# Kernel tuning notes

Measured on AMD Instinct MI355X. Metric: run time of the kernel, lower is better.

## Reference

```python
import jax, jax.numpy as jnp
import numpy as np

B = 4096          # batch
F = 1024          # feature_count * embedding_dim
E = 16            # embedding_dim (domain embedding)
D = 8             # num_domains
T = F + E         # cross-net total dim
L = 3             # cross layers
EPS = 1e-5


def setup_inputs() -> dict:
    key = jax.random.key(0)
    ks = jax.random.split(key, 32)
    s = 0.02
    inp = {}
    inp["x"] = jax.random.normal(ks[0], (B, F), dtype=jnp.float32)
    inp["domain_ids"] = jax.random.randint(ks[1], (B,), 0, D)
    # partitioned normalization params
    inp["pn_weight"] = jnp.ones((D, F), jnp.float32)
    inp["pn_bias"] = jnp.zeros((D, F), jnp.float32)
    # domain embedding table
    inp["dom_emb"] = jax.random.normal(ks[2], (D, E), jnp.float32) * 0.1
    # cross network: L layers, each Linear(T->1, no bias) + additive bias vector
    inp["cross_w"] = jax.random.normal(ks[3], (L, T), jnp.float32) * s
    inp["cross_b"] = jnp.zeros((L, T), jnp.float32)
    # center MLP: T->512->256->128 (ReLU, ReLU, none)
    inp["cW1"] = jax.random.normal(ks[4], (T, 512), jnp.float32) * s
    inp["cb1"] = jnp.zeros((512,), jnp.float32)
    inp["cW2"] = jax.random.normal(ks[5], (512, 256), jnp.float32) * s
    inp["cb2"] = jnp.zeros((256,), jnp.float32)
    inp["cW3"] = jax.random.normal(ks[6], (256, 128), jnp.float32) * s
    inp["cb3"] = jnp.zeros((128,), jnp.float32)
    # per-domain nets: T->512->256->128; last bias initialized to domain_net_init_bias=1.0
    inp["dW1"] = jax.random.normal(ks[7], (D, T, 512), jnp.float32) * s
    inp["db1"] = jnp.zeros((D, 512), jnp.float32)
    inp["dW2"] = jax.random.normal(ks[8], (D, 512, 256), jnp.float32) * s
    inp["db2"] = jnp.zeros((D, 256), jnp.float32)
    inp["dW3"] = jax.random.normal(ks[9], (D, 256, 128), jnp.float32) * s
    inp["db3"] = jnp.ones((D, 128), jnp.float32)
    # final MLP: 128->64->1
    inp["fW1"] = jax.random.normal(ks[10], (128, 64), jnp.float32) * s
    inp["fb1"] = jnp.zeros((64,), jnp.float32)
    inp["fW2"] = jax.random.normal(ks[11], (64, 1), jnp.float32) * s
    inp["fb2"] = jnp.zeros((1,), jnp.float32)
    # auxiliary net: E->32->1
    inp["aW1"] = jax.random.normal(ks[12], (E, 32), jnp.float32) * s
    inp["ab1"] = jnp.zeros((32,), jnp.float32)
    inp["aW2"] = jax.random.normal(ks[13], (32, 1), jnp.float32) * s
    inp["ab2"] = jnp.zeros((1,), jnp.float32)
    return inp


def _forward(x, domain_ids, pn_weight, pn_bias, dom_emb, cross_w, cross_b,
             cW1, cb1, cW2, cb2, cW3, cb3,
             dW1, db1, dW2, db2, dW3, db3,
             fW1, fb1, fW2, fb2, aW1, ab1, aW2, ab2):
    # --- PartitionedNormalization: per-sample LayerNorm stats + domain-indexed affine ---
    mean = jnp.mean(x, axis=1, keepdims=True)
    var = jnp.mean((x - mean) ** 2, axis=1, keepdims=True)  # unbiased=False
    normed = (x - mean) / jnp.sqrt(var + EPS)
    normed = normed * pn_weight[domain_ids] + pn_bias[domain_ids]

    xd = dom_emb[domain_ids]                    # (B, E)
    x0 = jnp.concatenate([normed, xd], axis=1)  # (B, T)

    # --- CrossNetworkWithDomain ---
    xc = x0
    for i in range(L):
        proj = xc @ cross_w[i]                  # (B,)
        xc = x0 * proj[:, None] + cross_b[i] + xc

    # --- center MLP ---
    h = jax.nn.relu(xc @ cW1 + cb1)
    h = jax.nn.relu(h @ cW2 + cb2)
    h_center = h @ cW3 + cb3                    # (B, 128)

    # --- domain-specific nets: run all D nets, select per-sample ---
    a = jax.nn.relu(jnp.einsum('bi,dio->bdo', xc, dW1) + db1[None])   # (B, D, 512)
    a = jax.nn.relu(jnp.einsum('bdi,dio->bdo', a, dW2) + db2[None])   # (B, D, 256)
    a = jnp.einsum('bdi,dio->bdo', a, dW3) + db3[None]                # (B, D, 128)
    h_domain = a[jnp.arange(a.shape[0]), domain_ids]                  # (B, 128)

    # --- STAR fusion (tanh) ---
    fused = h_center * jnp.tanh(h_domain)

    # --- final MLP + auxiliary net ---
    main_logits = jax.nn.relu(fused @ fW1 + fb1) @ fW2 + fb2          # (B, 1)
    aux_logits = jax.nn.relu(xd @ aW1 + ab1) @ aW2 + ab2              # (B, 1)
    return jax.nn.sigmoid(main_logits + aux_logits)


def reference(x, domain_ids, pn_weight, pn_bias, dom_emb, cross_w, cross_b,
              cW1, cb1, cW2, cb2, cW3, cb3,
              dW1, db1, dW2, db2, dW3, db3,
              fW1, fb1, fW2, fb2, aW1, ab1, aW2, ab2):
    return _forward(x, domain_ids, pn_weight, pn_bias, dom_emb, cross_w, cross_b,
                    cW1, cb1, cW2, cb2, cW3, cb3,
                    dW1, db1, dW2, db2, dW3, db3,
                    fW1, fb1, fW2, fb2, aW1, ab1, aW2, ab2)
```

## Files before the change

### kernel.cpp

```cpp
#include <hip/hip_runtime.h>
#include <math.h>
#include <stdint.h>

#define BATCH 4096
#define FEAT  1024
#define EDIM  16
#define NDOM  8
#define TDIM  1040
#define KP1   1088
#define NLAYER 3
#define EPSV  1e-5f

typedef __attribute__((ext_vector_type(8))) short bf16x8;
typedef __attribute__((ext_vector_type(4))) float f32x4;

__device__ __forceinline__ unsigned short f2bf(float f) {
    union { float f; unsigned int u; } v; v.f = f;
    unsigned int u = v.u;
    return (unsigned short)((u + 0x7fffu + ((u >> 16) & 1u)) >> 16);
}
__device__ __forceinline__ float bf2f(unsigned short u) {
    union { unsigned int u; float f; } v; v.u = ((unsigned int)u) << 16; return v.f;
}
__device__ __forceinline__ void gload_lds16(const void* g, void* l) {
    __builtin_amdgcn_global_load_lds(
        (const __attribute__((address_space(1))) void*)(g),
        (__attribute__((address_space(3))) void*)(l), 16, 0, 0);
}

#define T_W1 136
#define T_W2 32
#define T_W3 8
#define NCONV (T_W1*9 + T_W2*9 + T_W3*9)

__global__ __launch_bounds__(256) void front(
    const int* __restrict__ dom, int* __restrict__ perm, int* __restrict__ starts,
    const float* __restrict__ cW1, const float* __restrict__ dW1,
    const float* __restrict__ cW2, const float* __restrict__ dW2,
    const float* __restrict__ cW3, const float* __restrict__ dW3,
    unsigned short* __restrict__ Wc1b, unsigned short* __restrict__ Wd1b,
    unsigned short* __restrict__ Wc2b, unsigned short* __restrict__ Wd2b,
    unsigned short* __restrict__ Wc3b, unsigned short* __restrict__ Wd3b,
    const float* __restrict__ x,
    const float* __restrict__ pnw, const float* __restrict__ pnb,
    const float* __restrict__ demb,
    const float* __restrict__ crw, const float* __restrict__ crb,
    const float* __restrict__ aW1, const float* __restrict__ ab1,
    const float* __restrict__ aW2, const float* __restrict__ ab2,
    unsigned short* __restrict__ XCb, float* __restrict__ auxg) {
    int b = blockIdx.x;
    int t = threadIdx.x;

    if (b < NCONV) {
        __shared__ float tile[64][65];
        const float* src; unsigned short* dst; int K, N, Kp, rr;
        if (b < T_W1)            { src = cW1; dst = Wc1b; K = TDIM; N = 512; Kp = KP1; rr = b; }
        else if (b < T_W1*9)     { int r = b - T_W1; int z = r / T_W1; rr = r % T_W1;
                                   src = dW1 + (size_t)z * TDIM * 512; dst = Wd1b + (size_t)z * 512 * KP1;
                                   K = TDIM; N = 512; Kp = KP1; }
        else if (b < T_W1*9+T_W2)   { src = cW2; dst = Wc2b; K = 512; N = 256; Kp = 512; rr = b - T_W1*9; }
        else if (b < T_W1*9+T_W2*9) { int r = b - (T_W1*9+T_W2); int z = r / T_W2; rr = r % T_W2;
                                   src = dW2 + (size_t)z * 512 * 256; dst = Wd2b + (size_t)z * 256 * 512;
                                   K = 512; N = 256; Kp = 512; }
        else if (b < T_W1*9+T_W2*9+T_W3) { src = cW3; dst = Wc3b; K = 256; N = 128; Kp = 256; rr = b - (T_W1*9+T_W2*9); }
        else                     { int r = b - (T_W1*9+T_W2*9+T_W3); int z = r / T_W3; rr = r % T_W3;
                                   src = dW3 + (size_t)z * 256 * 128; dst = Wd3b + (size_t)z * 128 * 256;
                                   K = 256; N = 128; Kp = 256; }
        int kt = Kp >> 6;
        int kb = rr % kt, nb = rr / kt;
        int k0 = kb * 64, n0 = nb * 64;
        #pragma unroll
        for (int i = 0; i < 4; i++) {
            int flat = t + i * 256;
            int kr = flat >> 4, c4 = flat & 15;
            int k = k0 + kr;
            float4 v = make_float4(0.f, 0.f, 0.f, 0.f);
            if (k < K) v = *(const float4*)(src + (size_t)k * N + n0 + c4 * 4);
            tile[kr][c4 * 4 + 0] = v.x;
            tile[kr][c4 * 4 + 1] = v.y;
            tile[kr][c4 * 4 + 2] = v.z;
            tile[kr][c4 * 4 + 3] = v.w;
        }
        __syncthreads();
        #pragma unroll
        for (int i = 0; i < 4; i++) {
            int flat = t + i * 256;
            int n = flat >> 4, kg = flat & 15;
            ushort4 sv;
            sv.x = f2bf(tile[kg * 4 + 0][n]);
            sv.y = f2bf(tile[kg * 4 + 1][n]);
            sv.z = f2bf(tile[kg * 4 + 2][n]);
            sv.w = f2bf(tile[kg * 4 + 3][n]);
            *(ushort4*)(dst + (size_t)(n0 + n) * Kp + k0 + kg * 4) = sv;
        }
        return;
    }
    if (b == NCONV) {
        __shared__ int cnt[NDOM];
        __shared__ int off[NDOM];
        if (t < NDOM) cnt[t] = 0;
        __syncthreads();
        for (int i = t; i < BATCH; i += 256) atomicAdd(&cnt[dom[i]], 1);
        __syncthreads();
        if (t == 0) {
            int s = 0;
            for (int d = 0; d < NDOM; d++) { off[d] = s; starts[d] = s; s += cnt[d]; }
            starts[NDOM] = s;
        }
        __syncthreads();
        for (int i = t; i < BATCH; i += 256) {
            int p = atomicAdd(&off[dom[i]], 1);
            perm[p] = i;
        }
        return;
    }

    int w = t >> 6, lane = t & 63;
    int row = (b - NCONV - 1) * 4 + w;
    int d = dom[row];

    float4 X[4];
    #pragma unroll
    for (int j = 0; j < 4; j++)
        X[j] = *(const float4*)(x + (size_t)row * FEAT + 4 * lane + 256 * j);

    float s = 0.f, ss = 0.f;
    #pragma unroll
    for (int j = 0; j < 4; j++) {
        s  += X[j].x + X[j].y + X[j].z + X[j].w;
        ss += X[j].x*X[j].x + X[j].y*X[j].y + X[j].z*X[j].z + X[j].w*X[j].w;
    }
    #pragma unroll
    for (int m = 1; m < 64; m <<= 1) {
        s  += __shfl_xor(s,  m);
        ss += __shfl_xor(ss, m);
    }
    float mean = s / (float)FEAT;
    float var  = ss / (float)FEAT - mean * mean;
    float rstd = rsqrtf(var + EPSV);

    float4 x0[4], xc[4];
    #pragma unroll
    for (int j = 0; j < 4; j++) {
        float4 wv = *(const float4*)(pnw + (size_t)d * FEAT + 4 * lane + 256 * j);
        float4 bv = *(const float4*)(pnb + (size_t)d * FEAT + 4 * lane + 256 * j);
        x0[j].x = (X[j].x - mean) * rstd * wv.x + bv.x;
        x0[j].y = (X[j].y - mean) * rstd * wv.y + bv.y;
        x0[j].z = (X[j].z - mean) * rstd * wv.z + bv.z;
        x0[j].w = (X[j].w - mean) * rstd * wv.w + bv.w;
        xc[j] = x0[j];
    }
    float x0e = 0.f, xce = 0.f;
    if (lane < EDIM) { x0e = demb[d * EDIM + lane]; xce = x0e; }

    #pragma unroll
    for (int l = 0; l < NLAYER; l++) {
        const float* wl = crw + l * TDIM;
        const float* bl = crb + l * TDIM;
        float partial = 0.f;
        #pragma unroll
        for (int j = 0; j < 4; j++) {
            float4 wv = *(const float4*)(wl + 4 * lane + 256 * j);
            partial += xc[j].x*wv.x + xc[j].y*wv.y + xc[j].z*wv.z + xc[j].w*wv.w;
        }
        if (lane < EDIM) partial += xce * wl[FEAT + lane];
        #pragma unroll
        for (int m = 1; m < 64; m <<= 1) partial += __shfl_xor(partial, m);
        float proj = partial;
        #pragma unroll
        for (int j = 0; j < 4; j++) {
            float4 bv = *(const float4*)(bl + 4 * lane + 256 * j);
            xc[j].x = fmaf(x0[j].x, proj, bv.x + xc[j].x);
            xc[j].y = fmaf(x0[j].y, proj, bv.y + xc[j].y);
            xc[j].z = fmaf(x0[j].z, proj, bv.z + xc[j].z);
            xc[j].w = fmaf(x0[j].w, proj, bv.w + xc[j].w);
        }
        if (lane < EDIM) xce = fmaf(x0e, proj, bl[FEAT + lane] + xce);
    }

    #pragma unroll
    for (int j = 0; j < 4; j++) {
        ushort4 sv;
        sv.x = f2bf(xc[j].x); sv.y = f2bf(xc[j].y);
        sv.z = f2bf(xc[j].z); sv.w = f2bf(xc[j].w);
        *(ushort4*)(XCb + (size_t)row * KP1 + 4 * lane + 256 * j) = sv;
    }
    XCb[(size_t)row * KP1 + FEAT + lane] = (lane < EDIM) ? f2bf(xce) : 0;

    float h = (lane < 32) ? ab1[lane] : 0.f;
    #pragma unroll
    for (int e = 0; e < EDIM; e++) {
        float ev = __shfl(xce, e);
        if (lane < 32) h = fmaf(ev, aW1[e * 32 + lane], h);
    }
    float c = (lane < 32) ? fmaxf(h, 0.f) * aW2[lane] : 0.f;
    #pragma unroll
    for (int m = 1; m < 64; m <<= 1) c += __shfl_xor(c, m);
    if (lane == 0) auxg[row] = c + ab2[0];
}

__global__ __launch_bounds__(256) void gemm_l1_fused(
    const unsigned short* __restrict__ A,
    const unsigned short* __restrict__ Wc,
    const unsigned short* __restrict__ Wd,
    const float* __restrict__ bc, const float* __restrict__ bd,
    unsigned short* __restrict__ Cc, unsigned short* __restrict__ Cd,
    const int* __restrict__ starts, const int* __restrict__ perm) {
    __shared__ short As[2][64 * 64];
    __shared__ short Bs[2][128 * 64];

    int xb = blockIdx.x;
    int d = xb >> 4, sl = xb & 15;
    int ds = starts[d], de = starts[d + 1];
    int m0 = ds + sl * 64;
    if (m0 >= de) return;
    int mEnd = de;
    int n0 = blockIdx.y * 64;

    int tid = threadIdx.x;
    int w = tid >> 6, lane = tid & 63;
    int lr = lane & 15, q = lane >> 4;

    const unsigned short* pA[2]; int sA[2];
    const unsigned short* pB[4]; int sB[4];
    #pragma unroll
    for (int i = 0; i < 2; i++) {
        int seg = i * 4 + w;
        int ch = seg * 64 + lane;
        int loc = ch >> 3, c = ch & 7;
        int mm = m0 + loc; if (mm > mEnd - 1) mm = mEnd - 1;
        int rowp = perm[mm];
        pA[i] = A + (size_t)rowp * KP1 + ((c ^ (loc & 7)) << 3);
        sA[i] = seg * 512;
    }
    #pragma unroll
    for (int i = 0; i < 4; i++) {
        int seg = i * 4 + w;
        int ch = seg * 64 + lane;
        int loc = ch >> 3, c = ch & 7;
        const unsigned short* base = (loc < 64)
            ? (Wc + (size_t)(n0 + loc) * KP1)
            : (Wd + ((size_t)d * 512 + n0 + (loc - 64)) * KP1);
        pB[i] = base + ((c ^ (loc & 7)) << 3);
        sB[i] = seg * 512;
    }

    f32x4 acc[4][2];
    #pragma unroll
    for (int i = 0; i < 4; i++)
        #pragma unroll
        for (int j = 0; j < 2; j++)
            acc[i][j] = (f32x4){0.f, 0.f, 0.f, 0.f};

    #pragma unroll
    for (int i = 0; i < 2; i++) gload_lds16(pA[i], As[0] + sA[i]);
    #pragma unroll
    for (int i = 0; i < 4; i++) gload_lds16(pB[i], Bs[0] + sB[i]);
    __syncthreads();

    #pragma unroll 1
    for (int ks = 0; ks < KP1 / 64; ks++) {
        int cur = ks & 1, nxt = cur ^ 1;
        if (ks < KP1 / 64 - 1) {
            int k0 = (ks + 1) * 64;
            #pragma unroll
            for (int i = 0; i < 2; i++) gload_lds16(pA[i] + k0, As[nxt] + sA[i]);
            #pragma unroll
            for (int i = 0; i < 4; i++) gload_lds16(pB[i] + k0, Bs[nxt] + sB[i]);
        }
        #pragma unroll
        for (int half = 0; half < 2; half++) {
            int cc = half * 4 + q;
            bf16x8 af[4], bf[2];
            #pragma unroll
            for (int i = 0; i < 4; i++) {
                int m = i * 16 + lr;
                af[i] = *(const bf16x8*)(As[cur] + m * 64 + ((cc ^ (m & 7)) << 3));
            }
            #pragma unroll
            for (int j = 0; j < 2; j++) {
                int n = w * 32 + j * 16 + lr;
                bf[j] = *(const bf16x8*)(Bs[cur] + n * 64 + ((cc ^ (n & 7)) << 3));
            }
            #pragma unroll
            for (int i = 0; i < 4; i++)
                #pragma unroll
                for (int j = 0; j < 2; j++)
                    acc[i][j] = __builtin_amdgcn_mfma_f32_16x16x32_bf16(
                        af[i], bf[j], acc[i][j], 0, 0, 0);
        }
        __syncthreads();
    }

    int chain = w >> 1, hn = w & 1;
    const float* bias = chain ? (bd + d * 512) : bc;
    unsigned short* C = chain ? Cd : Cc;
    #pragma unroll
    for (int i = 0; i < 4; i++) {
        #pragma unroll
        for (int j = 0; j < 2; j++) {
            int col = n0 + hn * 32 + j * 16 + lr;
            float bvv = bias[col];
            int rowb = m0 + i * 16 + q * 4;
            #pragma unroll
            for (int r = 0; r < 4; r++) {
                int row = rowb + r;
                if (row >= mEnd) continue;
                C[(size_t)row * 512 + col] = f2bf(fmaxf(acc[i][j][r] + bvv, 0.f));
            }
        }
    }
}

__global__ __launch_bounds__(256) void tail_fused(
    const unsigned short* __restrict__ H1c, const unsigned short* __restrict__ H1d,
    const unsigned short* __restrict__ Wc2, const unsigned short* __restrict__ Wd2,
    const float* __restrict__ cb2v, const float* __restrict__ db2v,
    const unsigned short* __restrict__ Wc3, const unsigned short* __restrict__ Wd3,
    const float* __restrict__ cb3v, const float* __restrict__ db3v,
    const float* __restrict__ fW1, const float* __restrict__ fb1,
    const float* __restrict__ fW2, const float* __restrict__ fb2,
    const float* __restrict__ auxg, const int* __restrict__ perm,
    const int* __restrict__ starts, float* __restrict__ out) {

    __shared__ __align__(16) char smem[98304];
    short* Bsb[2] = { (short*)smem, (short*)(smem + 32768) };
    short* Asb[2] = { (short*)(smem + 65536), (short*)(smem + 69632) };
    short* H2    = (short*)(smem + 73728);
    short* fused = (short*)(smem + 90112);

    int y = blockIdx.x;
    int d = y & 7, sl = y >> 3;
    int ds = starts[d], de = starts[d + 1];
    int m0 = ds + sl * 32;
    if (m0 >= de) return;
    int mEnd = de;

    int tid = threadIdx.x;
    int w = tid >> 6, lane = tid & 63;
    int lr = lane & 15, q = lane >> 4;

    int bn = w * 8 + (lane >> 3);
    int sw = ((lane & 7) ^ (bn & 7)) << 3;
    int rowA = m0 + bn; if (rowA > mEnd - 1) rowA = mEnd - 1;

    const unsigned short* pA0  = H1c + (size_t)rowA * 512 + sw;
    const unsigned short* pA1  = H1d + (size_t)rowA * 512 + sw;
    const unsigned short* pW20 = Wc2 + (size_t)bn * 512 + sw;
    const unsigned short* pW21 = Wd2 + (size_t)d * 256 * 512 + (size_t)bn * 512 + sw;
    const unsigned short* pW30 = Wc3 + (size_t)bn * 256 + sw;
    const unsigned short* pW31 = Wd3 + (size_t)d * 128 * 256 + (size_t)bn * 256 + sw;

    auto stage_l2 = [&](int c, int k0, int pb) {
        const unsigned short* pa = c ? pA1 : pA0;
        const unsigned short* pw = c ? pW21 : pW20;
        gload_lds16(pa + k0, Asb[pb] + w * 512);
        #pragma unroll
        for (int i = 0; i < 8; i++)
            gload_lds16(pw + (size_t)i * 32 * 512 + k0, Bsb[pb] + (i * 4 + w) * 512);
    };
    auto stage_l3 = [&](int c, int k0, int pb) {
        const unsigned short* pw = c ? pW31 : pW30;
        #pragma unroll
        for (int i = 0; i < 4; i++)
            gload_lds16(pw + (size_t)i * 32 * 256 + k0, Bsb[pb] + (i * 4 + w) * 512);
    };

    stage_l2(0, 0, 0);
    __syncthreads();

    #pragma unroll
    for (int c = 0; c < 2; c++) {
        f32x4 acc2[2][4];
        #pragma unroll
        for (int i = 0; i < 2; i++)
            #pragma unroll
            for (int j = 0; j < 4; j++) acc2[i][j] = (f32x4){0.f, 0.f, 0.f, 0.f};

        #pragma unroll
        for (int it = 0; it < 8; it++) {
            int t = c * 12 + it;
            int pb = t & 1, pn = pb ^ 1;
            if (it < 7) stage_l2(c, (it + 1) * 64, pn);
            else        stage_l3(c, 0, pn);

            #pragma unroll
            for (int half = 0; half < 2; half++) {
                int cc = half * 4 + q;
                bf16x8 af[2], bf[4];
                #pragma unroll
                for (int i = 0; i < 2; i++) {
                    int m = i * 16 + lr;
                    af[i] = *(const bf16x8*)(Asb[pb] + m * 64 + ((cc ^ (m & 7)) << 3));
                }
                #pragma unroll
                for (int j = 0; j < 4; j++) {
                    int n = w * 64 + j * 16 + lr;
                    bf[j] = *(const bf16x8*)(Bsb[pb] + n * 64 + ((cc ^ (n & 7)) << 3));
                }
                #pragma unroll
                for (int i = 0; i < 2; i++)
                    #pragma unroll
                    for (int j = 0; j < 4; j++)
                        acc2[i][j] = __builtin_amdgcn_mfma_f32_16x16x32_bf16(
                            af[i], bf[j], acc2[i][j], 0, 0, 0);
            }
            __syncthreads();
        }

        const float* b2 = c ? (db2v + d * 256) : cb2v;
        #pragma unroll
        for (int i = 0; i < 2; i++)
            #pragma unroll
            for (int j = 0; j < 4; j++) {
                int col = w * 64 + j * 16 + lr;
                float bv = b2[col];
                int cch = col >> 3;
                #pragma unroll
                for (int r = 0; r < 4; r++) {
                    int row = i * 16 + q * 4 + r;
                    int pc = (cch & 24) | ((cch ^ (row & 7)) & 7);
                    float v = fmaxf(acc2[i][j][r] + bv, 0.f);
                    H2[row * 256 + pc * 8 + (col & 7)] = (short)f2bf(v);
                }
            }
        __syncthreads();

        f32x4 acc3[2][2];
        #pragma unroll
        for (int i = 0; i < 2; i++)
            #pragma unroll
            for (int j = 0; j < 2; j++) acc3[i][j] = (f32x4){0.f, 0.f, 0.f, 0.f};

        #pragma unroll
        for (int it = 0; it < 4; it++) {
            int t = c * 12 + 8 + it;
            int pb = t & 1, pn = pb ^ 1;
            if (it < 3)      stage_l3(c, (it + 1) * 64, pn);
            else if (c == 0) stage_l2(1, 0, pn);

            #pragma unroll
            for (int half = 0; half < 2; half++) {
                int cc = half * 4 + q;
                int C = it * 8 + cc;
                bf16x8 af[2], bf[2];
                #pragma unroll
                for (int i = 0; i < 2; i++) {
                    int m = i * 16 + lr;
                    int pcm = (C & 24) | ((C ^ (m & 7)) & 7);
                    af[i] = *(const bf16x8*)(H2 + m * 256 + pcm * 8);
                }
                #pragma unroll
                for (int j = 0; j < 2; j++) {
                    int n = w * 32 + j * 16 + lr;
                    bf[j] = *(const bf16x8*)(Bsb[pb] + n * 64 + ((cc ^ (n & 7)) << 3));
                }
                #pragma unroll
                for (int i = 0; i < 2; i++)
                    #pragma unroll
                    for (int j = 0; j < 2; j++)
                        acc3[i][j] = __builtin_amdgcn_mfma_f32_16x16x32_bf16(
                            af[i], bf[j], acc3[i][j], 0, 0, 0);
            }
            __syncthreads();
        }

        const float* b3 = c ? (db3v + d * 128) : cb3v;
        #pragma unroll
        for (int i = 0; i < 2; i++)
            #pragma unroll
            for (int j = 0; j < 2; j++) {
                int col = w * 32 + j * 16 + lr;
                float bv = b3[col];
                int cch = col >> 3;
                #pragma unroll
                for (int r = 0; r < 4; r++) {
                    int row = i * 16 + q * 4 + r;
                    int pc = (cch & 8) | ((cch ^ (row & 7)) & 7);
                    int idx = row * 128 + pc * 8 + (col & 7);
                    if (c == 0) {
                        fused[idx] = (short)f2bf(acc3[i][j][r] + bv);
                    } else {
                        float cv = bf2f((unsigned short)fused[idx]);
                        fused[idx] = (short)f2bf(cv * tanhf(acc3[i][j][r] + bv));
                    }
                }
            }
        __syncthreads();
    }

    short* Bsf = Bsb[0];
    float* Ls  = (float*)Asb[0];
    for (int s2 = tid; s2 < 1024; s2 += 256) {
        int n = s2 >> 4, cch = s2 & 15;
        bf16x8 vv;
        #pragma unroll
        for (int kk = 0; kk < 8; kk++)
            vv[kk] = (short)f2bf(fW1[(cch * 8 + kk) * 64 + n]);
        int pc = (cch & 8) | ((cch ^ (n & 7)) & 7);
        *(bf16x8*)(Bsf + n * 128 + pc * 8) = vv;
    }
    __syncthreads();

    int wm = w >> 1, wn = w & 1;
    f32x4 acc2f[2];
    #pragma unroll
    for (int j = 0; j < 2; j++) acc2f[j] = (f32x4){0.f, 0.f, 0.f, 0.f};
    #pragma unroll
    for (int g = 0; g < 4; g++) {
        int cc = g * 4 + q;
        int m = wm * 16 + lr;
        int pcm = (cc & 8) | ((cc ^ (m & 7)) & 7);
        bf16x8 af = *(const bf16x8*)(fused + m * 128 + pcm * 8);
        #pragma unroll
        for (int j = 0; j < 2; j++) {
            int n = wn * 32 + j * 16 + lr;
            int pcn = (cc & 8) | ((cc ^ (n & 7)) & 7);
            bf16x8 bf = *(const bf16x8*)(Bsf + n * 128 + pcn * 8);
            acc2f[j] = __builtin_amdgcn_mfma_f32_16x16x32_bf16(af, bf, acc2f[j], 0, 0, 0);
        }
    }

    float w2v[2], b1v[2];
    #pragma unroll
    for (int j = 0; j < 2; j++) {
        int col = wn * 32 + j * 16 + lr;
        w2v[j] = fW2[col];
        b1v[j] = fb1[col];
    }
    float rowv[4];
    #pragma unroll
    for (int r = 0; r < 4; r++) {
        float v = 0.f;
        #pragma unroll
        for (int j = 0; j < 2; j++)
            v += fmaxf(acc2f[j][r] + b1v[j], 0.f) * w2v[j];
        v += __shfl_xor(v, 1);
        v += __shfl_xor(v, 2);
        v += __shfl_xor(v, 4);
        v += __shfl_xor(v, 8);
        rowv[r] = v;
    }
    if (wn == 0 && lr == 0) {
        #pragma unroll
        for (int r = 0; r < 4; r++)
            Ls[wm * 16 + q * 4 + r] = rowv[r];
    }
    __syncthreads();
    if (wn == 1 && lr == 0) {
        float b2 = fb2[0];
        #pragma unroll
        for (int r = 0; r < 4; r++) {
            int row = wm * 16 + q * 4 + r;
            int p = m0 + row;
            if (p < mEnd) {
                int orow = perm[p];
                float logit = Ls[row] + rowv[r] + b2 + auxg[orow];
                out[orow] = 1.f / (1.f + expf(-logit));
            }
        }
    }
}

extern "C" void kernel_launch(void* const* d_in, const int* in_sizes, int n_in,
                              void* d_out, int out_size, void* d_ws, size_t ws_size,
                              hipStream_t stream) {
    (void)in_sizes; (void)n_in; (void)out_size; (void)ws_size;

    const float* x    = (const float*)d_in[0];
    const int*   dom  = (const int*)  d_in[1];
    const float* pnw  = (const float*)d_in[2];
    const float* pnb  = (const float*)d_in[3];
    const float* demb = (const float*)d_in[4];
    const float* crw  = (const float*)d_in[5];
    const float* crb  = (const float*)d_in[6];
    const float* cW1  = (const float*)d_in[7];
    const float* cb1  = (const float*)d_in[8];
    const float* cW2  = (const float*)d_in[9];
    const float* cb2  = (const float*)d_in[10];
    const float* cW3  = (const float*)d_in[11];
    const float* cb3  = (const float*)d_in[12];
    const float* dW1  = (const float*)d_in[13];
    const float* db1  = (const float*)d_in[14];
    const float* dW2  = (const float*)d_in[15];
    const float* db2  = (const float*)d_in[16];
    const float* dW3  = (const float*)d_in[17];
    const float* db3  = (const float*)d_in[18];
    const float* fW1  = (const float*)d_in[19];
    const float* fb1  = (const float*)d_in[20];
    const float* fW2  = (const float*)d_in[21];
    const float* fb2  = (const float*)d_in[22];
    const float* aW1  = (const float*)d_in[23];
    const float* ab1  = (const float*)d_in[24];
    const float* aW2  = (const float*)d_in[25];
    const float* ab2  = (const float*)d_in[26];
    float* out = (float*)d_out;

    char* base = (char*)d_ws;
    size_t o = 0;
    auto alloc = [&](size_t bytes) { char* p = base + o; o += (bytes + 255) & ~size_t(255); return p; };

    int* perm   = (int*)alloc(BATCH * 4);
    int* starts = (int*)alloc((NDOM + 1) * 4);
    float* auxg = (float*)alloc(BATCH * 4);
    unsigned short* XCb  = (unsigned short*)alloc((size_t)BATCH * KP1 * 2);
    unsigned short* H1c  = (unsigned short*)alloc((size_t)BATCH * 512 * 2);
    unsigned short* H1d  = (unsigned short*)alloc((size_t)BATCH * 512 * 2);
    unsigned short* Wc1b = (unsigned short*)alloc((size_t)512 * KP1 * 2);
    unsigned short* Wd1b = (unsigned short*)alloc((size_t)NDOM * 512 * KP1 * 2);
    unsigned short* Wc2b = (unsigned short*)alloc((size_t)256 * 512 * 2);
    unsigned short* Wd2b = (unsigned short*)alloc((size_t)NDOM * 256 * 512 * 2);
    unsigned short* Wc3b = (unsigned short*)alloc((size_t)128 * 256 * 2);
    unsigned short* Wd3b = (unsigned short*)alloc((size_t)NDOM * 128 * 256 * 2);

    front<<<NCONV + 1 + BATCH / 4, 256, 0, stream>>>(
        dom, perm, starts, cW1, dW1, cW2, dW2, cW3, dW3,
        Wc1b, Wd1b, Wc2b, Wd2b, Wc3b, Wd3b,
        x, pnw, pnb, demb, crw, crb, aW1, ab1, aW2, ab2, XCb, auxg);

    gemm_l1_fused<<<dim3(NDOM * 16, 8), 256, 0, stream>>>(
        XCb, Wc1b, Wd1b, cb1, db1, H1c, H1d, starts, perm);

    tail_fused<<<NDOM * 128, 256, 0, stream>>>(
        H1c, H1d, Wc2b, Wd2b, cb2, db2, Wc3b, Wd3b, cb3, db3,
        fW1, fb1, fW2, fb2, auxg, perm, starts, out);
}
```

Baseline: 197.9 us.

## Pipeline GEMM stages with explicit vmcnt waits and a two-step-ahead prefetch

The first-layer GEMM loop replaces __syncthreads with explicit s_waitcnt on vmcnt plus raw barriers and sched_barriers, so the next tile's async global-to-LDS loads can stay in flight across the barrier. The tail kernel flattens its layer-2/layer-3 chains into 24 uniform steps with two-deep prefetch and per-step vmcnt thresholds, and the buffer layout is reorganized. The blockIdx mapping for domain/slice is also changed to group blocks by domain. This aims to hide global load latency and drop redundant full waits, at the risk of subtle races if the hand-computed wait counts are wrong.

Measured after the change: 193.7 us. 1.02x faster.

```diff
diff --git a/kernel.cpp b/kernel.cpp
--- a/kernel.cpp
+++ b/kernel.cpp
@@ -13,6 +13,11 @@
 
 typedef __attribute__((ext_vector_type(8))) short bf16x8;
 typedef __attribute__((ext_vector_type(4))) float f32x4;
+
+#define VMW(N)  __builtin_amdgcn_s_waitcnt((((N)&15)|(((N)>>4)<<14)|(15<<8)|(7<<4)))
+#define LGKW0   __builtin_amdgcn_s_waitcnt((15|(3<<14)|(7<<4)))
+#define SBAR    __builtin_amdgcn_s_barrier()
+#define SCB     __builtin_amdgcn_sched_barrier(0)
 
 __device__ __forceinline__ unsigned short f2bf(float f) {
     union { float f; unsigned int u; } v; v.f = f;
@@ -256,7 +261,6 @@
     for (int i = 0; i < 2; i++) gload_lds16(pA[i], As[0] + sA[i]);
     #pragma unroll
     for (int i = 0; i < 4; i++) gload_lds16(pB[i], Bs[0] + sB[i]);
-    __syncthreads();
 
     #pragma unroll 1
     for (int ks = 0; ks < KP1 / 64; ks++) {
@@ -267,7 +271,11 @@
             for (int i = 0; i < 2; i++) gload_lds16(pA[i] + k0, As[nxt] + sA[i]);
             #pragma unroll
             for (int i = 0; i < 4; i++) gload_lds16(pB[i] + k0, Bs[nxt] + sB[i]);
-        }
+            VMW(6);
+        } else {
+            VMW(0);
+        }
+        SBAR; SCB;
         #pragma unroll
         for (int half = 0; half < 2; half++) {
             int cc = half * 4 + q;
@@ -289,7 +297,7 @@
                     acc[i][j] = __builtin_amdgcn_mfma_f32_16x16x32_bf16(
                         af[i], bf[j], acc[i][j], 0, 0, 0);
         }
-        __syncthreads();
+        LGKW0; SBAR; SCB;
     }
 
     int chain = w >> 1, hn = w & 1;
@@ -324,13 +332,17 @@
     const int* __restrict__ starts, float* __restrict__ out) {
 
     __shared__ __align__(16) char smem[98304];
-    short* Bsb[2] = { (short*)smem, (short*)(smem + 32768) };
-    short* Asb[2] = { (short*)(smem + 65536), (short*)(smem + 69632) };
+    short* BufB[2]; short* BufA[2];
+    #pragma unroll
+    for (int i = 0; i < 2; i++) {
+        BufB[i] = (short*)(smem + i * 36864);
+        BufA[i] = (short*)(smem + i * 36864 + 32768);
+    }
     short* H2    = (short*)(smem + 73728);
     short* fused = (short*)(smem + 90112);
 
     int y = blockIdx.x;
-    int d = y & 7, sl = y >> 3;
+    int d = y >> 7, sl = y & 127;
     int ds = starts[d], de = starts[d + 1];
     int m0 = ds + sl * 32;
     if (m0 >= de) return;
@@ -351,39 +363,36 @@
     const unsigned short* pW30 = Wc3 + (size_t)bn * 256 + sw;
     const unsigned short* pW31 = Wd3 + (size_t)d * 128 * 256 + (size_t)bn * 256 + sw;
 
-    auto stage_l2 = [&](int c, int k0, int pb) {
-        const unsigned short* pa = c ? pA1 : pA0;
-        const unsigned short* pw = c ? pW21 : pW20;
-        gload_lds16(pa + k0, Asb[pb] + w * 512);
-        #pragma unroll
-        for (int i = 0; i < 8; i++)
-            gload_lds16(pw + (size_t)i * 32 * 512 + k0, Bsb[pb] + (i * 4 + w) * 512);
+    auto istep = [&](int s) {
+        int c = s / 12, k = s % 12, b = s & 1;
+        if (k < 8) {
+            const unsigned short* pa = c ? pA1 : pA0;
+            const unsigned short* pw = c ? pW21 : pW20;
+            int k0 = k * 64;
+            gload_lds16(pa + k0, BufA[b] + w * 512);
+            #pragma unroll
+            for (int i = 0; i < 8; i++)
+                gload_lds16(pw + (size_t)i * 32 * 512 + k0, BufB[b] + (i * 4 + w) * 512);
+        } else {
+            const unsigned short* pw = c ? pW31 : pW30;
+            int k0 = (k - 8) * 64;
+            #pragma unroll
+            for (int i = 0; i < 4; i++)
+                gload_lds16(pw + (size_t)i * 32 * 256 + k0, BufB[b] + (i * 4 + w) * 512);
+        }
     };
-    auto stage_l3 = [&](int c, int k0, int pb) {
-        const unsigned short* pw = c ? pW31 : pW30;
-        #pragma unroll
-        for (int i = 0; i < 4; i++)
-            gload_lds16(pw + (size_t)i * 32 * 256 + k0, Bsb[pb] + (i * 4 + w) * 512);
-    };
-
-    stage_l2(0, 0, 0);
-    __syncthreads();
-
-    #pragma unroll
-    for (int c = 0; c < 2; c++) {
-        f32x4 acc2[2][4];
-        #pragma unroll
-        for (int i = 0; i < 2; i++)
-            #pragma unroll
-            for (int j = 0; j < 4; j++) acc2[i][j] = (f32x4){0.f, 0.f, 0.f, 0.f};
-
-        #pragma unroll
-        for (int it = 0; it < 8; it++) {
-            int t = c * 12 + it;
-            int pb = t & 1, pn = pb ^ 1;
-            if (it < 7) stage_l2(c, (it + 1) * 64, pn);
-            else        stage_l3(c, 0, pn);
-
+
+    f32x4 acc2[2][4], acc3[2][2];
+
+    auto cstep = [&](int s) {
+        int c = s / 12, k = s % 12, b = s & 1;
+        if (k < 8) {
+            if (k == 0) {
+                #pragma unroll
+                for (int i = 0; i < 2; i++)
+                    #pragma unroll
+                    for (int j = 0; j < 4; j++) acc2[i][j] = (f32x4){0.f, 0.f, 0.f, 0.f};
+            }
             #pragma unroll
             for (int half = 0; half < 2; half++) {
                 int cc = half * 4 + q;
@@ -391,12 +400,12 @@
                 #pragma unroll
                 for (int i = 0; i < 2; i++) {
                     int m = i * 16 + lr;
-                    af[i] = *(const bf16x8*)(Asb[pb] + m * 64 + ((cc ^ (m & 7)) << 3));
+                    af[i] = *(const bf16x8*)(BufA[b] + m * 64 + ((cc ^ (m & 7)) << 3));
                 }
                 #pragma unroll
                 for (int j = 0; j < 4; j++) {
                     int n = w * 64 + j * 16 + lr;
-                    bf[j] = *(const bf16x8*)(Bsb[pb] + n * 64 + ((cc ^ (n & 7)) << 3));
+                    bf[j] = *(const bf16x8*)(BufB[b] + n * 64 + ((cc ^ (n & 7)) << 3));
                 }
                 #pragma unroll
                 for (int i = 0; i < 2; i++)
@@ -405,40 +414,32 @@
                         acc2[i][j] = __builtin_amdgcn_mfma_f32_16x16x32_bf16(
                             af[i], bf[j], acc2[i][j], 0, 0, 0);
             }
-            __syncthreads();
-        }
-
-        const float* b2 = c ? (db2v + d * 256) : cb2v;
-        #pragma unroll
-        for (int i = 0; i < 2; i++)
-            #pragma unroll
-            for (int j = 0; j < 4; j++) {
-                int col = w * 64 + j * 16 + lr;
-                float bv = b2[col];
-                int cch = col >> 3;
-                #pragma unroll
-                for (int r = 0; r < 4; r++) {
-                    int row = i * 16 + q * 4 + r;
-                    int pc = (cch & 24) | ((cch ^ (row & 7)) & 7);
-                    float v = fmaxf(acc2[i][j][r] + bv, 0.f);
-                    H2[row * 256 + pc * 8 + (col & 7)] = (short)f2bf(v);
-                }
-            }
-        __syncthreads();
-
-        f32x4 acc3[2][2];
-        #pragma unroll
-        for (int i = 0; i < 2; i++)
-            #pragma unroll
-            for (int j = 0; j < 2; j++) acc3[i][j] = (f32x4){0.f, 0.f, 0.f, 0.f};
-
-        #pragma unroll
-        for (int it = 0; it < 4; it++) {
-            int t = c * 12 + 8 + it;
-            int pb = t & 1, pn = pb ^ 1;
-            if (it < 3)      stage_l3(c, (it + 1) * 64, pn);
-            else if (c == 0) stage_l2(1, 0, pn);
-
+            if (k == 7) {
+                const float* b2 = c ? (db2v + d * 256) : cb2v;
+                #pragma unroll
+                for (int i = 0; i < 2; i++)
+                    #pragma unroll
+                    for (int j = 0; j < 4; j++) {
+                        int col = w * 64 + j * 16 + lr;
+                        float bv = b2[col];
+                        int cch = col >> 3;
+                        #pragma unroll
+                        for (int r = 0; r < 4; r++) {
+                            int row = i * 16 + q * 4 + r;
+                            int pc = (cch & 24) | ((cch ^ (row & 7)) & 7);
+                            float v = fmaxf(acc2[i][j][r] + bv, 0.f);
+                            H2[row * 256 + pc * 8 + (col & 7)] = (short)f2bf(v);
+                        }
+                    }
+            }
+        } else {
+            int it = k - 8;
+            if (it == 0) {
+                #pragma unroll
+                for (int i = 0; i < 2; i++)
+                    #pragma unroll
+                    for (int j = 0; j < 2; j++) acc3[i][j] = (f32x4){0.f, 0.f, 0.f, 0.f};
+            }
             #pragma unroll
             for (int half = 0; half < 2; half++) {
                 int cc = half * 4 + q;
@@ -453,7 +454,7 @@
                 #pragma unroll
                 for (int j = 0; j < 2; j++) {
                     int n = w * 32 + j * 16 + lr;
-                    bf[j] = *(const bf16x8*)(Bsb[pb] + n * 64 + ((cc ^ (n & 7)) << 3));
+                    bf[j] = *(const bf16x8*)(BufB[b] + n * 64 + ((cc ^ (n & 7)) << 3));
                 }
                 #pragma unroll
                 for (int i = 0; i < 2; i++)
@@ -462,35 +463,53 @@
                         acc3[i][j] = __builtin_amdgcn_mfma_f32_16x16x32_bf16(
                             af[i], bf[j], acc3[i][j], 0, 0, 0);
             }
-            __syncthreads();
-        }
-
-        const float* b3 = c ? (db3v + d * 128) : cb3v;
-        #pragma unroll
-        for (int i = 0; i < 2; i++)
-            #pragma unroll
-            for (int j = 0; j < 2; j++) {
-                int col = w * 32 + j * 16 + lr;
-                float bv = b3[col];
-                int cch = col >> 3;
-                #pragma unroll
-                for (int r = 0; r < 4; r++) {
-                    int row = i * 16 + q * 4 + r;
-                    int pc = (cch & 8) | ((cch ^ (row & 7)) & 7);
-                    int idx = row * 128 + pc * 8 + (col & 7);
-                    if (c == 0) {
-                        fused[idx] = (short)f2bf(acc3[i][j][r] + bv);
-                    } else {
-                        float cv = bf2f((unsigned short)fused[idx]);
-                        fused[idx] = (short)f2bf(cv * tanhf(acc3[i][j][r] + bv));
+            if (it == 3) {
+                const float* b3 = c ? (db3v + d * 128) : cb3v;
+                #pragma unroll
+                for (int i = 0; i < 2; i++)
+                    #pragma unroll
+                    for (int j = 0; j < 2; j++) {
+                        int col = w * 32 + j * 16 + lr;
+                        float bv = b3[col];
+                        int cch = col >> 3;
+                        #pragma unroll
+                        for (int r = 0; r < 4; r++) {
+                            int row = i * 16 + q * 4 + r;
+                            int pc = (cch & 8) | ((cch ^ (row & 7)) & 7);
+                            int idx = row * 128 + pc * 8 + (col & 7);
+                            if (c == 0) {
+                                fused[idx] = (short)f2bf(acc3[i][j][r] + bv);
+                            } else {
+                                float cv = bf2f((unsigned short)fused[idx]);
+                                fused[idx] = (short)f2bf(cv * tanhf(acc3[i][j][r] + bv));
+                            }
+                        }
                     }
-                }
-            }
-        __syncthreads();
-    }
-
-    short* Bsf = Bsb[0];
-    float* Ls  = (float*)Asb[0];
+            }
+        }
+    };
+
+    #define TSTEP(S, NW) do { \
+        VMW(NW); SBAR; SCB; \
+        cstep(S); \
+        LGKW0; SBAR; SCB; \
+        if ((S) + 2 < 24) istep((S) + 2); \
+    } while (0)
+
+    istep(0); istep(1);
+
+    TSTEP(0, 9);   TSTEP(1, 9);   TSTEP(2, 9);   TSTEP(3, 9);
+    TSTEP(4, 9);   TSTEP(5, 9);   TSTEP(6, 9);   TSTEP(7, 4);
+    TSTEP(8, 4);   TSTEP(9, 4);   TSTEP(10, 4);  TSTEP(11, 9);
+    TSTEP(12, 9);  TSTEP(13, 9);  TSTEP(14, 9);  TSTEP(15, 9);
+    TSTEP(16, 9);  TSTEP(17, 9);  TSTEP(18, 9);  TSTEP(19, 4);
+    TSTEP(20, 4);  TSTEP(21, 4);  TSTEP(22, 4);  TSTEP(23, 0);
+    #undef TSTEP
+
+    __syncthreads();
+
+    short* Bsf = BufB[0];
+    float* Ls  = (float*)BufA[0];
     for (int s2 = tid; s2 < 1024; s2 += 256) {
         int n = s2 >> 4, cch = s2 & 15;
         bf16x8 vv;
```
